# Kernel optimization log

Hardware: AMD Instinct MI355X
Metric: run time of the kernel (lower is better)

## Reference

```python
import jax, jax.numpy as jnp
import numpy as np


def setup_inputs() -> dict:
    key = jax.random.key(0)
    k1, k2 = jax.random.split(key)
    N, D, C = 131072, 512, 1024
    logits = jax.random.normal(k1, (N, D), dtype=jnp.float32)
    labels = jax.random.randint(k2, (N,), 0, C, dtype=jnp.int32)
    return {"logits": logits, "labels": labels, "num_classes": C}


def reference(logits, labels, num_classes):
    # Row-wise L2 normalize (X = X / ||X||)
    Xn = logits / jnp.sqrt(jnp.sum(logits * logits, axis=-1, keepdims=True))
    # Per-class mean prototype W_c = mean over rows with label c, then renormalize
    ones = jnp.ones(labels.shape, dtype=Xn.dtype)
    counts = jax.ops.segment_sum(ones, labels, num_segments=num_classes)  # [C]
    sums = jax.ops.segment_sum(Xn, labels, num_segments=num_classes)      # [C, D]
    W = sums / jnp.maximum(counts, 1.0)[:, None]
    wnorm = jnp.sqrt(jnp.sum(W * W, axis=-1, keepdims=True))
    W = W / jnp.where(wnorm > 0, wnorm, 1.0)
    # Soft-target cross entropy per row: -sum_d W[label_i, d] * log_softmax(Xn_i)_d
    logp = jax.nn.log_softmax(Xn, axis=-1)          # [N, D]
    ce = -jnp.sum(W[labels] * logp, axis=-1)        # [N]
    # Per-class mean loss (matches nn.CrossEntropyLoss()(X_c, W_c.repeat) per group)
    loss_per_class = jax.ops.segment_sum(ce, labels, num_segments=num_classes) / jnp.maximum(counts, 1.0)
    return loss_per_class
```

## Files before the change

### kernel.cpp

```cpp
#include <hip/hip_runtime.h>

constexpr int D      = 512;
constexpr int C      = 1024;
constexpr int CAP    = 256;
constexpr int CHUNKS = 4;

__global__ __launch_bounds__(256) void scatter_kernel(
    const int* __restrict__ labels, int* __restrict__ cursor,
    int* __restrict__ bucket, int N)
{
    const int i = blockIdx.x * 256 + threadIdx.x;
    if (i < N) {
        const int l   = labels[i];
        const int pos = atomicAdd(&cursor[l], 1);
        bucket[l * CAP + pos] = i;
    }
}

__global__ __launch_bounds__(256, 8) void class_partial_kernel(
    const float* __restrict__ logits, const int* __restrict__ cursor,
    const int* __restrict__ bucket, float* __restrict__ part,
    float* __restrict__ lzpart)
{
    const int blk  = blockIdx.x;
    const int c    = blk >> 2;
    const int ch   = blk & 3;
    const int t    = threadIdx.x;
    const int wave = t >> 6;
    const int lane = t & 63;
    const int cnt  = cursor[c];
    const int w16  = ch * 4 + wave;
    const int* __restrict__ myb = bucket + c * CAP;

    float acc[8] = {0.f, 0.f, 0.f, 0.f, 0.f, 0.f, 0.f, 0.f};
    float logZ   = 0.f;

    int j = w16;
    for (; j + 16 < cnt; j += 32) {
        const int row0 = myb[j];
        const int row1 = myb[j + 16];
        const float4* p0 = (const float4*)(logits + (size_t)row0 * D);
        const float4* p1 = (const float4*)(logits + (size_t)row1 * D);
        float4 a0 = p0[lane], b0 = p0[lane + 64];
        float4 a1 = p1[lane], b1 = p1[lane + 64];
        float x0[8] = {a0.x, a0.y, a0.z, a0.w, b0.x, b0.y, b0.z, b0.w};
        float x1[8] = {a1.x, a1.y, a1.z, a1.w, b1.x, b1.y, b1.z, b1.w};

        float ss0 = 0.f, ss1 = 0.f;
#pragma unroll
        for (int k = 0; k < 8; ++k) { ss0 += x0[k] * x0[k]; ss1 += x1[k] * x1[k]; }
#pragma unroll
        for (int off = 32; off; off >>= 1) {
            ss0 += __shfl_xor(ss0, off, 64);
            ss1 += __shfl_xor(ss1, off, 64);
        }
        const float inv0 = rsqrtf(ss0);
        const float inv1 = rsqrtf(ss1);

        float e0 = 0.f, e1 = 0.f;
#pragma unroll
        for (int k = 0; k < 8; ++k) {
            e0 += __expf(x0[k] * inv0);
            e1 += __expf(x1[k] * inv1);
        }
#pragma unroll
        for (int off = 32; off; off >>= 1) {
            e0 += __shfl_xor(e0, off, 64);
            e1 += __shfl_xor(e1, off, 64);
        }
        logZ += __logf(e0) + __logf(e1);

#pragma unroll
        for (int k = 0; k < 8; ++k) acc[k] += x0[k] * inv0 + x1[k] * inv1;
    }
    for (; j < cnt; j += 16) {
        const int row0 = myb[j];
        const float4* p0 = (const float4*)(logits + (size_t)row0 * D);
        float4 a0 = p0[lane], b0 = p0[lane + 64];
        float x0[8] = {a0.x, a0.y, a0.z, a0.w, b0.x, b0.y, b0.z, b0.w};

        float ss0 = 0.f;
#pragma unroll
        for (int k = 0; k < 8; ++k) ss0 += x0[k] * x0[k];
#pragma unroll
        for (int off = 32; off; off >>= 1) ss0 += __shfl_xor(ss0, off, 64);
        const float inv0 = rsqrtf(ss0);

        float e0 = 0.f;
#pragma unroll
        for (int k = 0; k < 8; ++k) e0 += __expf(x0[k] * inv0);
#pragma unroll
        for (int off = 32; off; off >>= 1) e0 += __shfl_xor(e0, off, 64);
        logZ += __logf(e0);

#pragma unroll
        for (int k = 0; k < 8; ++k) acc[k] += x0[k] * inv0;
    }

    __shared__ float lacc[4][D];
    __shared__ float lzs[4];

    ((float4*)lacc[wave])[lane]      = make_float4(acc[0], acc[1], acc[2], acc[3]);
    ((float4*)lacc[wave])[lane + 64] = make_float4(acc[4], acc[5], acc[6], acc[7]);
    if (lane == 0) lzs[wave] = logZ;
    __syncthreads();

    float2 v0 = ((const float2*)lacc[0])[t];
    float2 v1 = ((const float2*)lacc[1])[t];
    float2 v2 = ((const float2*)lacc[2])[t];
    float2 v3 = ((const float2*)lacc[3])[t];
    const float ax = v0.x + v1.x + v2.x + v3.x;
    const float ay = v0.y + v1.y + v2.y + v3.y;

    ((float2*)(part + (size_t)blk * D))[t] = make_float2(ax, ay);
    if (t == 0) lzpart[blk] = lzs[0] + lzs[1] + lzs[2] + lzs[3];
}

__global__ __launch_bounds__(256) void finalize_kernel(
    const float* __restrict__ part, const float* __restrict__ lzpart,
    const int* __restrict__ cursor, float* __restrict__ out)
{
    const int c    = blockIdx.x;
    const int t    = threadIdx.x;
    const int wave = t >> 6;
    const int lane = t & 63;

    float2 a = ((const float2*)(part + (size_t)(4 * c + 0) * D))[t];
    float2 b = ((const float2*)(part + (size_t)(4 * c + 1) * D))[t];
    float2 g = ((const float2*)(part + (size_t)(4 * c + 2) * D))[t];
    float2 h = ((const float2*)(part + (size_t)(4 * c + 3) * D))[t];
    const float ax = a.x + b.x + g.x + h.x;
    const float ay = a.y + b.y + g.y + h.y;

    float ssp = ax * ax + ay * ay;
    float smp = ax + ay;
#pragma unroll
    for (int off = 32; off; off >>= 1) {
        ssp += __shfl_xor(ssp, off, 64);
        smp += __shfl_xor(smp, off, 64);
    }

    __shared__ float2 red2[4];
    if (lane == 0) red2[wave] = make_float2(ssp, smp);
    __syncthreads();

    if (t == 0) {
        const float sstot = red2[0].x + red2[1].x + red2[2].x + red2[3].x;
        const float smtot = red2[0].y + red2[1].y + red2[2].y + red2[3].y;
        const float lzsum = lzpart[4 * c] + lzpart[4 * c + 1]
                          + lzpart[4 * c + 2] + lzpart[4 * c + 3];
        const int   cnt   = cursor[c];
        float loss = 0.f;
        if (cnt > 0 && sstot > 0.f) {
            const float nrm = sqrtf(sstot);
            loss = -(nrm - lzsum * (smtot / nrm)) / (float)cnt;
        }
        out[c] = loss;
    }
}

extern "C" void kernel_launch(void* const* d_in, const int* in_sizes, int n_in,
                              void* d_out, int out_size, void* d_ws, size_t ws_size,
                              hipStream_t stream)
{
    const float* logits = (const float*)d_in[0];
    const int*   labels = (const int*)d_in[1];
    const int N = in_sizes[1];

    char* w = (char*)d_ws;
    int*   cursor = (int*)w;   w += C * 4;
    int*   bucket = (int*)w;   w += (size_t)C * CAP * 4;
    float* part   = (float*)w; w += (size_t)C * CHUNKS * D * 4;
    float* lzpart = (float*)w; w += C * CHUNKS * 4;

    hipMemsetAsync(cursor, 0, C * 4, stream);

    scatter_kernel<<<(N + 255) / 256, 256, 0, stream>>>(labels, cursor, bucket, N);
    class_partial_kernel<<<C * CHUNKS, 256, 0, stream>>>(logits, cursor, bucket, part, lzpart);
    finalize_kernel<<<C, 256, 0, stream>>>(part, lzpart, cursor, (float*)d_out);
}
```

Measured before the change: 86.32 us.

## Use DPP wave reductions and nontemporal loads in class partial kernel

```diff
diff --git a/kernel.cpp b/kernel.cpp
--- a/kernel.cpp
+++ b/kernel.cpp
@@ -4,6 +4,26 @@
 constexpr int C      = 1024;
 constexpr int CAP    = 256;
 constexpr int CHUNKS = 4;
+
+typedef float f32x4 __attribute__((ext_vector_type(4)));
+
+#define DPP_STEP(v, CTRL)                                                      \
+    do {                                                                       \
+        int _s = __builtin_amdgcn_update_dpp(0, __float_as_int(v), (CTRL),     \
+                                             0xF, 0xF, true);                  \
+        (v) += __int_as_float(_s);                                             \
+    } while (0)
+
+__device__ __forceinline__ float wave_sum_dpp(float v)
+{
+    DPP_STEP(v, 0xB1);
+    DPP_STEP(v, 0x4E);
+    DPP_STEP(v, 0x141);
+    DPP_STEP(v, 0x140);
+    DPP_STEP(v, 0x142);
+    DPP_STEP(v, 0x143);
+    return __int_as_float(__builtin_amdgcn_readlane(__float_as_int(v), 63));
+}
 
 __global__ __launch_bounds__(256) void scatter_kernel(
     const int* __restrict__ labels, int* __restrict__ cursor,
@@ -17,7 +37,7 @@
     }
 }
 
-__global__ __launch_bounds__(256, 8) void class_partial_kernel(
+__global__ __launch_bounds__(256, 6) void class_partial_kernel(
     const float* __restrict__ logits, const int* __restrict__ cursor,
     const int* __restrict__ bucket, float* __restrict__ part,
     float* __restrict__ lzpart)
@@ -39,23 +59,20 @@
     for (; j + 16 < cnt; j += 32) {
         const int row0 = myb[j];
         const int row1 = myb[j + 16];
-        const float4* p0 = (const float4*)(logits + (size_t)row0 * D);
-        const float4* p1 = (const float4*)(logits + (size_t)row1 * D);
-        float4 a0 = p0[lane], b0 = p0[lane + 64];
-        float4 a1 = p1[lane], b1 = p1[lane + 64];
+        const f32x4* p0 = (const f32x4*)(logits + (size_t)row0 * D);
+        const f32x4* p1 = (const f32x4*)(logits + (size_t)row1 * D);
+        f32x4 a0 = __builtin_nontemporal_load(p0 + lane);
+        f32x4 b0 = __builtin_nontemporal_load(p0 + lane + 64);
+        f32x4 a1 = __builtin_nontemporal_load(p1 + lane);
+        f32x4 b1 = __builtin_nontemporal_load(p1 + lane + 64);
         float x0[8] = {a0.x, a0.y, a0.z, a0.w, b0.x, b0.y, b0.z, b0.w};
         float x1[8] = {a1.x, a1.y, a1.z, a1.w, b1.x, b1.y, b1.z, b1.w};
 
         float ss0 = 0.f, ss1 = 0.f;
 #pragma unroll
         for (int k = 0; k < 8; ++k) { ss0 += x0[k] * x0[k]; ss1 += x1[k] * x1[k]; }
-#pragma unroll
-        for (int off = 32; off; off >>= 1) {
-            ss0 += __shfl_xor(ss0, off, 64);
-            ss1 += __shfl_xor(ss1, off, 64);
-        }
-        const float inv0 = rsqrtf(ss0);
-        const float inv1 = rsqrtf(ss1);
+        const float inv0 = rsqrtf(wave_sum_dpp(ss0));
+        const float inv1 = rsqrtf(wave_sum_dpp(ss1));
 
         float e0 = 0.f, e1 = 0.f;
 #pragma unroll
@@ -63,35 +80,27 @@
             e0 += __expf(x0[k] * inv0);
             e1 += __expf(x1[k] * inv1);
         }
-#pragma unroll
-        for (int off = 32; off; off >>= 1) {
-            e0 += __shfl_xor(e0, off, 64);
-            e1 += __shfl_xor(e1, off, 64);
-        }
-        logZ += __logf(e0) + __logf(e1);
+        logZ += __logf(wave_sum_dpp(e0)) + __logf(wave_sum_dpp(e1));
 
 #pragma unroll
         for (int k = 0; k < 8; ++k) acc[k] += x0[k] * inv0 + x1[k] * inv1;
     }
     for (; j < cnt; j += 16) {
         const int row0 = myb[j];
-        const float4* p0 = (const float4*)(logits + (size_t)row0 * D);
-        float4 a0 = p0[lane], b0 = p0[lane + 64];
+        const f32x4* p0 = (const f32x4*)(logits + (size_t)row0 * D);
+        f32x4 a0 = __builtin_nontemporal_load(p0 + lane);
+        f32x4 b0 = __builtin_nontemporal_load(p0 + lane + 64);
         float x0[8] = {a0.x, a0.y, a0.z, a0.w, b0.x, b0.y, b0.z, b0.w};
 
         float ss0 = 0.f;
 #pragma unroll
         for (int k = 0; k < 8; ++k) ss0 += x0[k] * x0[k];
-#pragma unroll
-        for (int off = 32; off; off >>= 1) ss0 += __shfl_xor(ss0, off, 64);
-        const float inv0 = rsqrtf(ss0);
+        const float inv0 = rsqrtf(wave_sum_dpp(ss0));
 
         float e0 = 0.f;
 #pragma unroll
         for (int k = 0; k < 8; ++k) e0 += __expf(x0[k] * inv0);
-#pragma unroll
-        for (int off = 32; off; off >>= 1) e0 += __shfl_xor(e0, off, 64);
-        logZ += __logf(e0);
+        logZ += __logf(wave_sum_dpp(e0));
 
 #pragma unroll
         for (int k = 0; k < 8; ++k) acc[k] += x0[k] * inv0;
@@ -173,7 +182,7 @@
     float* part   = (float*)w; w += (size_t)C * CHUNKS * D * 4;
     float* lzpart = (float*)w; w += C * CHUNKS * 4;
 
-    hipMemsetAsync(cursor, 0, C * 4, stream);
+    (void)hipMemsetAsync(cursor, 0, C * 4, stream);
 
     scatter_kernel<<<(N + 255) / 256, 256, 0, stream>>>(labels, cursor, bucket, N);
     class_partial_kernel<<<C * CHUNKS, 256, 0, stream>>>(logits, cursor, bucket, part, lzpart);
```

New measurement: 90.73 us. 5.1% more time.
